# Optimization experiments

Measured on AMD Instinct MI355X. Metric: run time of the kernel, lower is better.

## Reference

```python
import jax, jax.numpy as jnp
import numpy as np

B, M, P, A, D = 128, 64, 1024, 21, 64


def setup_inputs() -> dict:
    key = jax.random.key(0)
    ks = jax.random.split(key, 10)
    positions = jax.random.randint(ks[0], (B, M), 0, P)
    amino_acids = jax.random.randint(ks[1], (B, M), 0, A)
    # Embedding tables (torch nn.Embedding init ~ N(0,1))
    pos_table = jax.random.normal(ks[2], (P, D), dtype=jnp.float32)
    aa_table = jax.random.normal(ks[3], (A, D), dtype=jnp.float32)
    # 3-layer MLP: Linear(2D->D), GELU, Linear(D->D), GELU, Linear(D->1)
    W1 = jax.random.normal(ks[4], (2 * D, D), dtype=jnp.float32) / np.sqrt(2 * D)
    b1 = jnp.zeros((D,), dtype=jnp.float32)
    W2 = jax.random.normal(ks[5], (D, D), dtype=jnp.float32) / np.sqrt(D)
    b2 = jnp.zeros((D,), dtype=jnp.float32)
    W3 = jax.random.normal(ks[6], (D, 1), dtype=jnp.float32) / np.sqrt(D)
    b3 = jnp.zeros((1,), dtype=jnp.float32)
    return dict(positions=positions, amino_acids=amino_acids,
                pos_table=pos_table, aa_table=aa_table,
                W1=W1, b1=b1, W2=W2, b2=b2, W3=W3, b3=b3)


def reference(positions, amino_acids, pos_table, aa_table, W1, b1, W2, b2, W3, b3):
    n_pos = pos_table.shape[0]
    n_aa = aa_table.shape[0]
    b, m = positions.shape
    d = pos_table.shape[1]
    # Gather + combine embeddings: [b, m, d]
    e = pos_table[jnp.clip(positions, 0, n_pos - 1)] + aa_table[jnp.clip(amino_acids, 0, n_aa - 1)]
    # All ordered pairs (i, j): concat(e_i, e_j) -> [b, m, m, 2d]
    ei = jnp.broadcast_to(e[:, :, None, :], (b, m, m, d))
    ej = jnp.broadcast_to(e[:, None, :, :], (b, m, m, d))
    pair = jnp.concatenate([ei, ej], axis=-1)
    # Batched 3-layer MLP (exact GELU, matching torch default)
    h = jax.nn.gelu(pair @ W1 + b1, approximate=False)
    h = jax.nn.gelu(h @ W2 + b2, approximate=False)
    s = (h @ W3 + b3)[..., 0]  # [b, m, m]
    # Original computes score only for i < j with order (e_i, e_j) and mirrors;
    # diagonal stays zero.
    upper = jnp.triu(s, k=1)
    return upper + jnp.swapaxes(upper, -1, -2)
```

## Files before the change

### kernel.cpp

```cpp
#include <hip/hip_runtime.h>
#include <hip/hip_bf16.h>
#include <cmath>

#define BB 128
#define MM 64
#define DD 64
#define PP 1024
#define AN 21
#define UVP 68

typedef __attribute__((ext_vector_type(8))) short bf16x8;
typedef __attribute__((ext_vector_type(4))) float f32x4;

__device__ __forceinline__ float gelu_fast(float x) {
    const float p = fmaf(0.044715f * x * x, x, x);
    const float z = __builtin_amdgcn_exp2f(2.3022150322f * p);
    const float r = __builtin_amdgcn_rcpf(z + 1.0f);
    return fmaf(-x, r, x);
}

__device__ __forceinline__ unsigned pk2bf(float lo, float hi) {
    __hip_bfloat162 t = __float22bfloat162_rn(make_float2(lo, hi));
    unsigned u; __builtin_memcpy(&u, &t, 4);
    return u;
}

__device__ __forceinline__ float row_sum16(float x) {
    int t;
    t = __builtin_amdgcn_update_dpp(0, __float_as_int(x), 0xB1, 0xF, 0xF, true);
    x += __int_as_float(t);
    t = __builtin_amdgcn_update_dpp(0, __float_as_int(x), 0x4E, 0xF, 0xF, true);
    x += __int_as_float(t);
    t = __builtin_amdgcn_update_dpp(0, __float_as_int(x), 0x141, 0xF, 0xF, true);
    x += __int_as_float(t);
    t = __builtin_amdgcn_update_dpp(0, __float_as_int(x), 0x140, 0xF, 0xF, true);
    x += __int_as_float(t);
    return x;
}

__global__ __launch_bounds__(256) void k_fused(
    const int* __restrict__ positions, const int* __restrict__ amino,
    const float* __restrict__ pos_table, const float* __restrict__ aa_table,
    const float* __restrict__ W1, const float* __restrict__ b1,
    const float* __restrict__ W2, const float* __restrict__ b2,
    const float* __restrict__ W3, const float* __restrict__ b3,
    float* __restrict__ out)
{
    __shared__ __align__(16) float us[16][UVP];
    __shared__ __align__(16) float vs[16][UVP];
    const int lane = threadIdx.x & 63;
    const int wave = threadIdx.x >> 6;
    const int r = lane & 15;
    const int g = lane >> 4;

    const int blk = blockIdx.x;
    const int b   = blockIdx.y;
    const int ib = (0x1A211200u >> (3 * blk)) & 7;
    const int jb = (0x1A21B4D1u >> (3 * blk)) & 7;
    const bool diag = (blk >= 6);

    bf16x8 bfr[2][4];
#pragma unroll
    for (int kh = 0; kh < 2; ++kh)
#pragma unroll
        for (int cb = 0; cb < 4; ++cb) {
            const float* src = W2 + (kh * 32 + g * 8) * DD + cb * 16 + r;
            float t[8];
#pragma unroll
            for (int e = 0; e < 8; ++e) t[e] = src[e * DD];
            union { bf16x8 v8; unsigned u4[4]; } cvt;
            cvt.u4[0] = pk2bf(t[0], t[1]); cvt.u4[1] = pk2bf(t[2], t[3]);
            cvt.u4[2] = pk2bf(t[4], t[5]); cvt.u4[3] = pk2bf(t[6], t[7]);
            bfr[kh][cb] = cvt.v8;
        }
    float b2f[4], w3f[4];
#pragma unroll
    for (int cb = 0; cb < 4; ++cb) {
        b2f[cb] = b2[cb * 16 + r];
        w3f[cb] = W3[cb * 16 + r];
    }
    const float b3s = b3[0];

    if (wave < 2) {
        const int uv = wave;
        const int tb = uv ? jb : ib;

        bf16x8 w1f[2][4];
#pragma unroll
        for (int kh = 0; kh < 2; ++kh)
#pragma unroll
            for (int cb = 0; cb < 4; ++cb) {
                const float* src = W1 + (uv * DD + kh * 32 + g * 8) * DD + cb * 16 + r;
                float t[8];
#pragma unroll
                for (int e = 0; e < 8; ++e) t[e] = src[e * DD];
                union { bf16x8 v8; unsigned u4[4]; } cvt;
                cvt.u4[0] = pk2bf(t[0], t[1]); cvt.u4[1] = pk2bf(t[2], t[3]);
                cvt.u4[2] = pk2bf(t[4], t[5]); cvt.u4[3] = pk2bf(t[6], t[7]);
                w1f[kh][cb] = cvt.v8;
            }
        float b1f[4] = {0.0f, 0.0f, 0.0f, 0.0f};
        if (!uv) {
#pragma unroll
            for (int cb = 0; cb < 4; ++cb) b1f[cb] = b1[cb * 16 + r];
        }

        const int tok = b * MM + tb * 16 + r;
        int p = positions[tok];
        p = p < 0 ? 0 : (p > PP - 1 ? PP - 1 : p);
        int a = amino[tok];
        a = a < 0 ? 0 : (a > AN - 1 ? AN - 1 : a);

        bf16x8 ef[2];
#pragma unroll
        for (int kh = 0; kh < 2; ++kh) {
            const int koff = kh * 32 + g * 8;
            const float4 p0 = *(const float4*)(pos_table + p * DD + koff);
            const float4 p1 = *(const float4*)(pos_table + p * DD + koff + 4);
            const float4 a0 = *(const float4*)(aa_table + a * DD + koff);
            const float4 a1 = *(const float4*)(aa_table + a * DD + koff + 4);
            union { bf16x8 v8; unsigned u4[4]; } cvt;
            cvt.u4[0] = pk2bf(p0.x + a0.x, p0.y + a0.y);
            cvt.u4[1] = pk2bf(p0.z + a0.z, p0.w + a0.w);
            cvt.u4[2] = pk2bf(p1.x + a1.x, p1.y + a1.y);
            cvt.u4[3] = pk2bf(p1.z + a1.z, p1.w + a1.w);
            ef[kh] = cvt.v8;
        }

        float (* __restrict__ dst)[UVP] = uv ? vs : us;
#pragma unroll
        for (int cb = 0; cb < 4; ++cb) {
            f32x4 z = {0.0f, 0.0f, 0.0f, 0.0f};
            z = __builtin_amdgcn_mfma_f32_16x16x32_bf16(ef[0], w1f[0][cb], z, 0, 0, 0);
            z = __builtin_amdgcn_mfma_f32_16x16x32_bf16(ef[1], w1f[1][cb], z, 0, 0, 0);
#pragma unroll
            for (int reg = 0; reg < 4; ++reg)
                dst[g * 4 + reg][cb * 16 + r] = z[reg] + b1f[cb];
        }
    }

    __syncthreads();

    float* __restrict__ ob = out + b * (MM * MM);
    const int i0 = ib * 16;

#pragma unroll
    for (int tt = 0; tt < 4; ++tt) {
        const int pj = tt * 4 + wave;
        const int jg = jb * 16 + pj;

        bf16x8 afr[2];
#pragma unroll
        for (int kh = 0; kh < 2; ++kh) {
            const int koff = kh * 32 + g * 8;
            const float4 u0 = *(const float4*)&us[r][koff];
            const float4 u1 = *(const float4*)&us[r][koff + 4];
            const float4 v0 = *(const float4*)&vs[pj][koff];
            const float4 v1 = *(const float4*)&vs[pj][koff + 4];
            float x[8];
            x[0] = u0.x + v0.x; x[1] = u0.y + v0.y; x[2] = u0.z + v0.z; x[3] = u0.w + v0.w;
            x[4] = u1.x + v1.x; x[5] = u1.y + v1.y; x[6] = u1.z + v1.z; x[7] = u1.w + v1.w;
            unsigned w0 = pk2bf(gelu_fast(x[0]), gelu_fast(x[1]));
            unsigned w1 = pk2bf(gelu_fast(x[2]), gelu_fast(x[3]));
            unsigned w2 = pk2bf(gelu_fast(x[4]), gelu_fast(x[5]));
            unsigned w3 = pk2bf(gelu_fast(x[6]), gelu_fast(x[7]));
            union { bf16x8 v8; unsigned u4[4]; } cvt;
            cvt.u4[0] = w0; cvt.u4[1] = w1; cvt.u4[2] = w2; cvt.u4[3] = w3;
            afr[kh] = cvt.v8;
        }

        f32x4 acc[4];
#pragma unroll
        for (int cb = 0; cb < 4; ++cb) {
            f32x4 z = {0.0f, 0.0f, 0.0f, 0.0f};
            z = __builtin_amdgcn_mfma_f32_16x16x32_bf16(afr[0], bfr[0][cb], z, 0, 0, 0);
            acc[cb] = __builtin_amdgcn_mfma_f32_16x16x32_bf16(afr[1], bfr[1][cb], z, 0, 0, 0);
        }

        float s0, s1, s2, s3;
        {
            float a0 = 0, a1 = 0, a2 = 0, a3 = 0;
#pragma unroll
            for (int cb = 0; cb < 4; ++cb) {
                a0 = fmaf(gelu_fast(acc[cb][0] + b2f[cb]), w3f[cb], a0);
                a1 = fmaf(gelu_fast(acc[cb][1] + b2f[cb]), w3f[cb], a1);
                a2 = fmaf(gelu_fast(acc[cb][2] + b2f[cb]), w3f[cb], a2);
                a3 = fmaf(gelu_fast(acc[cb][3] + b2f[cb]), w3f[cb], a3);
            }
            s0 = row_sum16(a0) + b3s;
            s1 = row_sum16(a1) + b3s;
            s2 = row_sum16(a2) + b3s;
            s3 = row_sum16(a3) + b3s;
        }

        if (r < 4) {
            const int p = g * 4 + r;
            if (!diag || p <= pj) {
                float sc = (r == 0) ? s0 : (r == 1) ? s1 : (r == 2) ? s2 : s3;
                if (diag && p == pj) sc = 0.0f;
                const int ig = i0 + p;
                ob[ig * MM + jg] = sc;
                ob[jg * MM + ig] = sc;
            }
        }
    }
}

extern "C" void kernel_launch(void* const* d_in, const int* in_sizes, int n_in,
                              void* d_out, int out_size, void* d_ws, size_t ws_size,
                              hipStream_t stream) {
    const int*   positions = (const int*)  d_in[0];
    const int*   amino     = (const int*)  d_in[1];
    const float* pos_table = (const float*)d_in[2];
    const float* aa_table  = (const float*)d_in[3];
    const float* W1        = (const float*)d_in[4];
    const float* b1        = (const float*)d_in[5];
    const float* W2        = (const float*)d_in[6];
    const float* b2        = (const float*)d_in[7];
    const float* W3        = (const float*)d_in[8];
    const float* b3        = (const float*)d_in[9];
    float* out = (float*)d_out;

    k_fused<<<dim3(10, 128), 256, 0, stream>>>(positions, amino, pos_table,
                                               aa_table, W1, b1, W2, b2, W3, b3,
                                               out);
}
```

Measured before the change: 28.24 us.

## Pack pairs of diagonal triangle tiles into one block to avoid wasted work

The four diagonal 16x16 tiles previously each used a full block and computed all 256 pairs even though only the strict upper triangle is kept. The kernel now packs two diagonal tiles' triangles into one 16x16 work grid (triangle-packing), so 8 blocks per batch replace 10, and all four waves compute layer-1 projections for both diagonal tiles. The diagonal is zeroed explicitly. This cuts redundant MFMA and GELU work and the block count, in exchange for more complex index math and extra shared memory.

```diff
diff --git a/kernel.cpp b/kernel.cpp
--- a/kernel.cpp
+++ b/kernel.cpp
@@ -46,8 +46,7 @@
     const float* __restrict__ W3, const float* __restrict__ b3,
     float* __restrict__ out)
 {
-    __shared__ __align__(16) float us[16][UVP];
-    __shared__ __align__(16) float vs[16][UVP];
+    __shared__ __align__(16) float tiles[4][16][UVP];
     const int lane = threadIdx.x & 63;
     const int wave = threadIdx.x >> 6;
     const int r = lane & 15;
@@ -55,9 +54,11 @@
 
     const int blk = blockIdx.x;
     const int b   = blockIdx.y;
-    const int ib = (0x1A211200u >> (3 * blk)) & 7;
-    const int jb = (0x1A21B4D1u >> (3 * blk)) & 7;
-    const bool diag = (blk >= 6);
+    const bool packed = (blk >= 6);
+    const int ib = (0x11200u >> (3 * blk)) & 7;
+    const int jb = (0x1B4D1u >> (3 * blk)) & 7;
+    const int dlo = packed ? 2 * (blk - 6) : 0;
+    const int dhi = dlo + 1;
 
     bf16x8 bfr[2][4];
 #pragma unroll
@@ -81,9 +82,11 @@
     }
     const float b3s = b3[0];
 
-    if (wave < 2) {
-        const int uv = wave;
-        const int tb = uv ? jb : ib;
+    float* __restrict__ ob = out + b * (MM * MM);
+
+    if (packed || wave < 2) {
+        const int uv = wave & 1;
+        const int tb = packed ? (dlo + (wave >> 1)) : (uv ? jb : ib);
 
         bf16x8 w1f[2][4];
 #pragma unroll
@@ -127,7 +130,7 @@
             ef[kh] = cvt.v8;
         }
 
-        float (* __restrict__ dst)[UVP] = uv ? vs : us;
+        float (* __restrict__ dst)[UVP] = tiles[wave];
 #pragma unroll
         for (int cb = 0; cb < 4; ++cb) {
             f32x4 z = {0.0f, 0.0f, 0.0f, 0.0f};
@@ -139,24 +142,38 @@
         }
     }
 
+    if (packed && threadIdx.x < 32) {
+        const int m = dlo * 16 + threadIdx.x;
+        ob[m * (MM + 1)] = 0.0f;
+    }
+
     __syncthreads();
 
-    float* __restrict__ ob = out + b * (MM * MM);
-    const int i0 = ib * 16;
-
 #pragma unroll
     for (int tt = 0; tt < 4; ++tt) {
-        const int pj = tt * 4 + wave;
-        const int jg = jb * 16 + pj;
+        const int ss = tt * 4 + wave;
+
+        const float* up;
+        const float* vp;
+        int s = ss;
+        if (packed) {
+            s = ss ? ss : 8;
+            const bool lo = r < s;
+            up = lo ? &tiles[0][r][0]     : &tiles[2][r - s][0];
+            vp = lo ? &tiles[1][s][0]     : &tiles[3][16 - s][0];
+        } else {
+            up = &tiles[0][r][0];
+            vp = &tiles[1][ss][0];
+        }
 
         bf16x8 afr[2];
 #pragma unroll
         for (int kh = 0; kh < 2; ++kh) {
             const int koff = kh * 32 + g * 8;
-            const float4 u0 = *(const float4*)&us[r][koff];
-            const float4 u1 = *(const float4*)&us[r][koff + 4];
-            const float4 v0 = *(const float4*)&vs[pj][koff];
-            const float4 v1 = *(const float4*)&vs[pj][koff + 4];
+            const float4 u0 = *(const float4*)(up + koff);
+            const float4 u1 = *(const float4*)(up + koff + 4);
+            const float4 v0 = *(const float4*)(vp + koff);
+            const float4 v1 = *(const float4*)(vp + koff + 4);
             float x[8];
             x[0] = u0.x + v0.x; x[1] = u0.y + v0.y; x[2] = u0.z + v0.z; x[3] = u0.w + v0.w;
             x[4] = u1.x + v1.x; x[5] = u1.y + v1.y; x[6] = u1.z + v1.z; x[7] = u1.w + v1.w;
@@ -195,13 +212,18 @@
 
         if (r < 4) {
             const int p = g * 4 + r;
-            if (!diag || p <= pj) {
-                float sc = (r == 0) ? s0 : (r == 1) ? s1 : (r == 2) ? s2 : s3;
-                if (diag && p == pj) sc = 0.0f;
-                const int ig = i0 + p;
-                ob[ig * MM + jg] = sc;
-                ob[jg * MM + ig] = sc;
+            const float sc = (r == 0) ? s0 : (r == 1) ? s1 : (r == 2) ? s2 : s3;
+            int ig, jg;
+            if (packed) {
+                const bool lo = p < s;
+                ig = lo ? dlo * 16 + p : dhi * 16 + (p - s);
+                jg = lo ? dlo * 16 + s : dhi * 16 + (16 - s);
+            } else {
+                ig = ib * 16 + p;
+                jg = jb * 16 + ss;
             }
+            ob[ig * MM + jg] = sc;
+            ob[jg * MM + ig] = sc;
         }
     }
 }
@@ -221,7 +243,7 @@
     const float* b3        = (const float*)d_in[9];
     float* out = (float*)d_out;
 
-    k_fused<<<dim3(10, 128), 256, 0, stream>>>(positions, amino, pos_table,
-                                               aa_table, W1, b1, W2, b2, W3, b3,
-                                               out);
-}
+    k_fused<<<dim3(8, 128), 256, 0, stream>>>(positions, amino, pos_table,
+                                              aa_table, W1, b1, W2, b2, W3, b3,
+                                              out);
+}
```

Result: faster. 25.33 us (-10.3%).
